# Kernel optimization log

Hardware: AMD Instinct MI355X
Metric: run time of the kernel (lower is better)

Reference implementation:

```python
import jax, jax.numpy as jnp
import numpy as np

NEG_SLOPE = 0.2
BN_EPS = 1e-5


def _gat_conv(x, src, dst, W, a_src, a_dst, b, n_nodes):
    # PyG GATConv, heads=1: linear, per-edge leaky-relu score, per-dst softmax, scatter-add.
    h = x @ W  # [N, C]
    e = jax.nn.leaky_relu((h @ a_src)[src] + (h @ a_dst)[dst], NEG_SLOPE)  # [E]
    m = jax.ops.segment_max(e, dst, num_segments=n_nodes)
    m = jnp.where(jnp.isfinite(m), m, 0.0)  # nodes with no in-edges
    w = jnp.exp(e - m[dst])
    denom = jax.ops.segment_sum(w, dst, num_segments=n_nodes)
    alpha = w / (denom[dst] + 1e-16)  # [E]
    out = jax.ops.segment_sum(alpha[:, None] * h[src], dst, num_segments=n_nodes)
    return out + b


def setup_inputs() -> dict:
    key = jax.random.key(0)
    N, E, Q, C = 50000, 800000, 200000, 128
    ks = jax.random.split(key, 12)
    sc = 1.0 / np.sqrt(C)
    d = {
        "embedding": jax.random.normal(ks[0], (N, C), jnp.float32) * 0.1,
        "W1": jax.random.normal(ks[1], (C, C), jnp.float32) * sc,
        "a_src1": jax.random.normal(ks[2], (C,), jnp.float32) * sc,
        "a_dst1": jax.random.normal(ks[3], (C,), jnp.float32) * sc,
        "b1": jnp.zeros((C,), jnp.float32),
        "gamma": jnp.ones((C,), jnp.float32),
        "beta": jnp.zeros((C,), jnp.float32),
        "rmean": jnp.zeros((C,), jnp.float32),
        "rvar": jnp.ones((C,), jnp.float32),
        "W2": jax.random.normal(ks[4], (C, C), jnp.float32) * sc,
        "a_src2": jax.random.normal(ks[5], (C,), jnp.float32) * sc,
        "a_dst2": jax.random.normal(ks[6], (C,), jnp.float32) * sc,
        "b2": jnp.zeros((C,), jnp.float32),
        "Wp1": jax.random.normal(ks[7], (C, C), jnp.float32) * sc,
        "bp1": jnp.zeros((C,), jnp.float32),
        "Wp2": jax.random.normal(ks[8], (C, 1), jnp.float32) * sc,
        "bp2": jnp.zeros((1,), jnp.float32),
        "edge_index": jax.random.randint(ks[9], (2, E), 0, N, jnp.int32),
        "edges": jax.random.randint(ks[10], (2, Q), 0, N, jnp.int32),
    }
    return d


def reference(embedding, W1, a_src1, a_dst1, b1, gamma, beta, rmean, rvar,
              W2, a_src2, a_dst2, b2, Wp1, bp1, Wp2, bp2, edge_index, edges):
    N = embedding.shape[0]
    src, dst = edge_index[0], edge_index[1]
    # conv0 -> BN (eval, running stats) -> ReLU (dropout inactive in eval)
    x = _gat_conv(embedding, src, dst, W1, a_src1, a_dst1, b1, N)
    x = (x - rmean) * jax.lax.rsqrt(rvar + BN_EPS) * gamma + beta
    x = jax.nn.relu(x)
    # final conv
    x = _gat_conv(x, src, dst, W2, a_src2, a_dst2, b2, N)
    # LinkPredictor: elementwise product of endpoint embeddings -> MLP -> sigmoid
    h = x[edges[0]] * x[edges[1]]  # [Q, C]
    h = jax.nn.relu(h @ Wp1 + bp1)
    out = jax.nn.sigmoid(h @ Wp2 + bp2)
    return out[:, 0]
```

## Files before the change

kernel.cpp:

```cpp
#include <hip/hip_runtime.h>
#include <hip/hip_bf16.h>
#include <math.h>
#include <stdint.h>
#include <string.h>

#define NEG_SLOPE 0.2f
#define BN_EPS 1e-5f

typedef __attribute__((ext_vector_type(8))) short short8;
typedef __attribute__((ext_vector_type(4))) float float4v;

static __device__ __forceinline__ unsigned short f2bf(float f) {
    union { float f; unsigned u; } v; v.f = f;
    unsigned r = (v.u + 0x7fffu + ((v.u >> 16) & 1u)) >> 16;
    return (unsigned short)r;
}
static __device__ __forceinline__ float bf2f(unsigned short u) {
    union { unsigned u; float f; } v; v.u = ((unsigned)u) << 16;
    return v.f;
}

__global__ __launch_bounds__(256) void prep_all(
    const float* __restrict__ W1, const float* __restrict__ W2,
    const float* __restrict__ Wp1,
    unsigned short* __restrict__ wt1, unsigned short* __restrict__ wt2,
    unsigned short* __restrict__ wtp,
    const float* __restrict__ gamma, const float* __restrict__ beta,
    const float* __restrict__ rmean, const float* __restrict__ rvar,
    float* __restrict__ bnsc, float* __restrict__ bnsh,
    int* __restrict__ bcur, int nz) {
    int b = blockIdx.x;
    if (b < 192) {
        const float* W = (b < 64) ? W1 : (b < 128) ? W2 : Wp1;
        unsigned short* WT = (b < 64) ? wt1 : (b < 128) ? wt2 : wtp;
        int idx = (b & 63) * 256 + threadIdx.x;
        int k = idx >> 7, n = idx & 127;
        WT[n * 128 + k] = f2bf(W[idx]);
    } else {
        if (threadIdx.x < 128) {
            int c = threadIdx.x;
            float s = gamma[c] * rsqrtf(rvar[c] + BN_EPS);
            bnsc[c] = s;
            bnsh[c] = beta[c] - rmean[c] * s;
        }
        for (int i = threadIdx.x; i < nz; i += 256) bcur[i] = 0;
    }
}

#define BK_CAP 8192
#define BK_EPB 4096
#define BK_LDS 6144

__global__ __launch_bounds__(256) void bucket_scatter(const int* __restrict__ src,
                                                      const int* __restrict__ dst,
                                                      int* __restrict__ bcur,
                                                      unsigned long long* __restrict__ bucket,
                                                      int E) {
    __shared__ int lcnt[256];
    __shared__ int lbase[256];
    int t = threadIdx.x;
    int e0 = blockIdx.x * BK_EPB;
    lcnt[t] = 0;
    __syncthreads();

    int es[16], ed[16];
#pragma unroll
    for (int u = 0; u < 16; ++u) {
        int i = e0 + u * 256 + t;
        if (i < E) {
            es[u] = src[i];
            ed[u] = dst[i];
            atomicAdd(&lcnt[ed[u] >> 8], 1);
        } else {
            ed[u] = -1;
        }
    }
    __syncthreads();
    int c = lcnt[t];
    if (c > 0) lbase[t] = atomicAdd(&bcur[t], c);
    __syncthreads();
    lcnt[t] = 0;
    __syncthreads();
#pragma unroll
    for (int u = 0; u < 16; ++u) {
        if (ed[u] >= 0) {
            int bin = ed[u] >> 8;
            int r = atomicAdd(&lcnt[bin], 1);
            int slot = lbase[bin] + r;
            if (slot < BK_CAP)
                bucket[(size_t)bin * BK_CAP + slot] =
                    ((unsigned long long)(ed[u] & 255) << 32) | (unsigned)es[u];
        }
    }
}

__global__ __launch_bounds__(256) void bucket_offs_fill(
    const int* __restrict__ bcur,
    const unsigned long long* __restrict__ bucket,
    int* __restrict__ gcnt,
    int* __restrict__ offs, int* __restrict__ ends,
    int* __restrict__ csr, int N) {
    __shared__ unsigned long long rec[BK_LDS];
    __shared__ int cnt[256];
    __shared__ int sc[256];
    __shared__ int bbase;
    int t = threadIdx.x, b = blockIdx.x;
    const unsigned long long* gb = &bucket[(size_t)b * BK_CAP];
    cnt[t] = 0;
    int c = bcur[b];
    if (c > BK_CAP) c = BK_CAP;
    if (t == 0) bbase = atomicAdd(gcnt, c);
    int lim = (c < BK_LDS) ? c : BK_LDS;
    for (int i = t; i < lim; i += 256) rec[i] = gb[i];
    __syncthreads();
    for (int i = t; i < c; i += 256) {
        unsigned long long v = (i < BK_LDS) ? rec[i] : gb[i];
        atomicAdd(&cnt[(int)(v >> 32)], 1);
    }
    __syncthreads();
    int v = cnt[t];
    sc[t] = v;
    __syncthreads();
    for (int d = 1; d < 256; d <<= 1) {
        int u = (t >= d) ? sc[t - d] : 0;
        __syncthreads();
        sc[t] += u;
        __syncthreads();
    }
    int myoff = bbase + sc[t] - v;
    int node = (b << 8) + t;
    if (node < N) {
        offs[node] = myoff;
        ends[node] = myoff + v;
    }
    cnt[t] = myoff;
    __syncthreads();
    for (int i = t; i < c; i += 256) {
        unsigned long long rv = (i < BK_LDS) ? rec[i] : gb[i];
        int dl = (int)(rv >> 32);
        int s = (int)(rv & 0xffffffffu);
        int r = atomicAdd(&cnt[dl], 1);
        csr[r] = s;
    }
}

#define LP_RS 136

template <bool BF16_IN>
__global__ __launch_bounds__(256) void gemm_mfma(
    const void* __restrict__ Xv,
    const unsigned short* __restrict__ WT,
    const float* __restrict__ a_src, const float* __restrict__ a_dst,
    unsigned short* __restrict__ H,
    float* __restrict__ s_src, float* __restrict__ s_dst, int N)
{
    __shared__ unsigned short sA[128 * LP_RS];
    __shared__ unsigned short sW[128 * LP_RS];
    const float* Xf = (const float*)Xv;
    const unsigned short* Xh = (const unsigned short*)Xv;
    int tid = threadIdx.x;
    int r0 = blockIdx.x * 128;

#pragma unroll
    for (int it = 0; it < 8; ++it) {
        int idx = it * 2048 + tid * 8;
        int n = idx >> 7, k = idx & 127;
        *(short8*)&sW[n * LP_RS + k] = *(const short8*)&WT[idx];
    }
#pragma unroll
    for (int it = 0; it < 16; ++it) {
        int r = it * 8 + (tid >> 5);
        int c = (tid & 31) * 4;
        int row = r0 + r;
        ushort4 u = make_ushort4(0, 0, 0, 0);
        if (row < N) {
            if (BF16_IN) {
                u = *(const ushort4*)&Xh[(size_t)row * 128 + c];
            } else {
                float4 x = *(const float4*)&Xf[(size_t)row * 128 + c];
                u.x = f2bf(x.x); u.y = f2bf(x.y); u.z = f2bf(x.z); u.w = f2bf(x.w);
            }
        }
        *(ushort4*)&sA[r * LP_RS + c] = u;
    }
    __syncthreads();

    int wave = tid >> 6, lane = tid & 63;
    int ln = lane & 15, quad = lane >> 4;
    int rowbase = wave * 32;

    short8 af[2][4];
#pragma unroll
    for (int m = 0; m < 2; ++m)
#pragma unroll
        for (int kt = 0; kt < 4; ++kt)
            af[m][kt] = *(const short8*)&sA[(rowbase + m * 16 + ln) * LP_RS + kt * 32 + quad * 8];

    float4v acc[2][8];
#pragma unroll
    for (int m = 0; m < 2; ++m)
#pragma unroll
        for (int n = 0; n < 8; ++n)
            acc[m][n] = float4v{0.f, 0.f, 0.f, 0.f};

#pragma unroll
    for (int n = 0; n < 8; ++n) {
#pragma unroll
        for (int kt = 0; kt < 4; ++kt) {
            short8 bf = *(const short8*)&sW[(n * 16 + ln) * LP_RS + kt * 32 + quad * 8];
            acc[0][n] = __builtin_amdgcn_mfma_f32_16x16x32_bf16(af[0][kt], bf, acc[0][n], 0, 0, 0);
            acc[1][n] = __builtin_amdgcn_mfma_f32_16x16x32_bf16(af[1][kt], bf, acc[1][n], 0, 0, 0);
        }
    }

    float asr[8], adr[8];
#pragma unroll
    for (int n = 0; n < 8; ++n) {
        asr[n] = a_src[n * 16 + ln];
        adr[n] = a_dst[n * 16 + ln];
    }
#pragma unroll
    for (int m = 0; m < 2; ++m) {
        int rb = r0 + rowbase + m * 16 + quad * 4;
#pragma unroll
        for (int n = 0; n < 8; ++n) {
            int col = n * 16 + ln;
            float4v a = acc[m][n];
            if (rb + 0 < N) H[(size_t)(rb + 0) * 128 + col] = f2bf(a[0]);
            if (rb + 1 < N) H[(size_t)(rb + 1) * 128 + col] = f2bf(a[1]);
            if (rb + 2 < N) H[(size_t)(rb + 2) * 128 + col] = f2bf(a[2]);
            if (rb + 3 < N) H[(size_t)(rb + 3) * 128 + col] = f2bf(a[3]);
        }
#pragma unroll
        for (int r = 0; r < 4; ++r) {
            float ps = 0.f, pd = 0.f;
#pragma unroll
            for (int n = 0; n < 8; ++n) {
                float v = acc[m][n][r];
                ps = fmaf(v, asr[n], ps);
                pd = fmaf(v, adr[n], pd);
            }
#pragma unroll
            for (int o = 1; o < 16; o <<= 1) {
                ps += __shfl_xor(ps, o);
                pd += __shfl_xor(pd, o);
            }
            int row = rb + r;
            if (ln == 0 && row < N) { s_src[row] = ps; s_dst[row] = pd; }
        }
    }
}

__global__ __launch_bounds__(256) void gat_gather(const unsigned short* __restrict__ H,
                                                  const int* __restrict__ offs,
                                                  const int* __restrict__ ends,
                                                  const int* __restrict__ csr,
                                                  const float* __restrict__ s_src,
                                                  const float* __restrict__ s_dst,
                                                  const float* __restrict__ bias,
                                                  const float* __restrict__ bn_scale,
                                                  const float* __restrict__ bn_shift,
                                                  int do_bn_relu,
                                                  unsigned short* __restrict__ out, int N) {
    int wave = threadIdx.x >> 6, lane = threadIdx.x & 63;
    int half = lane >> 5, hl = lane & 31;
    int node = blockIdx.x * 8 + wave * 2 + half;
    if (node >= N) return;
    int c0 = hl * 4;
    int beg = offs[node], end = ends[node];
    float sd = s_dst[node];

    float a0 = 0.f, a1 = 0.f, a2 = 0.f, a3 = 0.f;
    float sw = 0.f;
    for (int chunk = beg; chunk < end; chunk += 32) {
        int i = chunk + hl;
        int sidx = 0;
        float w = 0.f;
        if (i < end) {
            sidx = csr[i];
            float e = s_src[sidx] + sd;
            e = (e >= 0.f) ? e : NEG_SLOPE * e;
            w = expf(e);
        }
        sw += w;
        int cnt = end - chunk;
        if (cnt > 32) cnt = 32;
        int u = 0;
        for (; u + 8 <= cnt; u += 8) {
            int s[8]; float ww[8]; ushort4 hv[8];
#pragma unroll
            for (int j = 0; j < 8; ++j) {
                s[j]  = __shfl(sidx, u + j, 32);
                ww[j] = __shfl(w, u + j, 32);
            }
#pragma unroll
            for (int j = 0; j < 8; ++j)
                hv[j] = *(const ushort4*)&H[(size_t)s[j] * 128 + c0];
#pragma unroll
            for (int j = 0; j < 8; ++j) {
                a0 = fmaf(ww[j], bf2f(hv[j].x), a0);
                a1 = fmaf(ww[j], bf2f(hv[j].y), a1);
                a2 = fmaf(ww[j], bf2f(hv[j].z), a2);
                a3 = fmaf(ww[j], bf2f(hv[j].w), a3);
            }
        }
        for (; u + 4 <= cnt; u += 4) {
            int s[4]; float ww[4]; ushort4 hv[4];
#pragma unroll
            for (int j = 0; j < 4; ++j) {
                s[j]  = __shfl(sidx, u + j, 32);
                ww[j] = __shfl(w, u + j, 32);
            }
#pragma unroll
            for (int j = 0; j < 4; ++j)
                hv[j] = *(const ushort4*)&H[(size_t)s[j] * 128 + c0];
#pragma unroll
            for (int j = 0; j < 4; ++j) {
                a0 = fmaf(ww[j], bf2f(hv[j].x), a0);
                a1 = fmaf(ww[j], bf2f(hv[j].y), a1);
                a2 = fmaf(ww[j], bf2f(hv[j].z), a2);
                a3 = fmaf(ww[j], bf2f(hv[j].w), a3);
            }
        }
        for (; u < cnt; ++u) {
            int sj = __shfl(sidx, u, 32);
            float wj = __shfl(w, u, 32);
            ushort4 hv = *(const ushort4*)&H[(size_t)sj * 128 + c0];
            a0 = fmaf(wj, bf2f(hv.x), a0);
            a1 = fmaf(wj, bf2f(hv.y), a1);
            a2 = fmaf(wj, bf2f(hv.z), a2);
            a3 = fmaf(wj, bf2f(hv.w), a3);
        }
    }
#pragma unroll
    for (int o = 16; o; o >>= 1) sw += __shfl_xor(sw, o);
    float inv = 1.f / (sw + 1e-16f);

    float o0 = a0 * inv + bias[c0 + 0];
    float o1 = a1 * inv + bias[c0 + 1];
    float o2 = a2 * inv + bias[c0 + 2];
    float o3 = a3 * inv + bias[c0 + 3];
    if (do_bn_relu) {
        o0 = fmaxf(o0 * bn_scale[c0 + 0] + bn_shift[c0 + 0], 0.f);
        o1 = fmaxf(o1 * bn_scale[c0 + 1] + bn_shift[c0 + 1], 0.f);
        o2 = fmaxf(o2 * bn_scale[c0 + 2] + bn_shift[c0 + 2], 0.f);
        o3 = fmaxf(o3 * bn_scale[c0 + 3] + bn_shift[c0 + 3], 0.f);
    }
    ushort4 ov;
    ov.x = f2bf(o0); ov.y = f2bf(o1); ov.z = f2bf(o2); ov.w = f2bf(o3);
    *(ushort4*)&out[(size_t)node * 128 + c0] = ov;
}

__global__ __launch_bounds__(512) void link_pred_mfma(
    const unsigned short* __restrict__ X,
    const int* __restrict__ E0, const int* __restrict__ E1,
    const unsigned short* __restrict__ WTg,
    const float* __restrict__ bp1,
    const float* __restrict__ Wp2,
    const float* __restrict__ bp2_p,
    float* __restrict__ out, int Q)
{
    __shared__ unsigned short sW[128 * LP_RS];
    int tid = threadIdx.x;
    int wave = tid >> 6, lane = tid & 63;
    int ln = lane & 15, quad = lane >> 4;

    int tile = blockIdx.x * 8 + wave;
    int qbase = tile * 32;

    int ea[2], eb[2];
#pragma unroll
    for (int m = 0; m < 2; ++m) {
        int q = qbase + m * 16 + ln;
        if (q >= Q) q = Q - 1;
        ea[m] = E0[q];
        eb[m] = E1[q];
    }

#pragma unroll
    for (int it = 0; it < 4; ++it) {
        int idx = it * 4096 + tid * 8;
        int n = idx >> 7, k = idx & 127;
        *(short8*)&sW[n * LP_RS + k] = *(const short8*)&WTg[idx];
    }

    short8 ra[2][4], rb[2][4];
#pragma unroll
    for (int m = 0; m < 2; ++m) {
        const unsigned short* pa = &X[(size_t)ea[m] * 128 + quad * 8];
        const unsigned short* pb = &X[(size_t)eb[m] * 128 + quad * 8];
#pragma unroll
        for (int kt = 0; kt < 4; ++kt) {
            ra[m][kt] = *(const short8*)(pa + kt * 32);
            rb[m][kt] = *(const short8*)(pb + kt * 32);
        }
    }

    float bias[8], w2c[8];
#pragma unroll
    for (int n = 0; n < 8; ++n) {
        bias[n] = bp1[n * 16 + ln];
        w2c[n] = Wp2[n * 16 + ln];
    }
    float b2 = bp2_p[0];

    __syncthreads();

    short8 af[2][4];
#pragma unroll
    for (int m = 0; m < 2; ++m) {
#pragma unroll
        for (int kt = 0; kt < 4; ++kt) {
            short8 p;
#pragma unroll
            for (int j = 0; j < 8; j += 2) {
                float p0 = bf2f((unsigned short)ra[m][kt][j]) *
                           bf2f((unsigned short)rb[m][kt][j]);
                float p1 = bf2f((unsigned short)ra[m][kt][j + 1]) *
                           bf2f((unsigned short)rb[m][kt][j + 1]);
                __hip_bfloat162 h2 = __float22bfloat162_rn(make_float2(p0, p1));
                unsigned pr;
                memcpy(&pr, &h2, 4);
                p[j]     = (short)(pr & 0xffffu);
                p[j + 1] = (short)(pr >> 16);
            }
            af[m][kt] = p;
        }
    }

    float r0[2] = {0.f, 0.f}, r1[2] = {0.f, 0.f}, r2[2] = {0.f, 0.f}, r3[2] = {0.f, 0.f};
#pragma unroll
    for (int n = 0; n < 8; ++n) {
        float4v a0 = float4v{bias[n], bias[n], bias[n], bias[n]};
        float4v a1 = a0;
#pragma unroll
        for (int kt = 0; kt < 4; ++kt) {
            short8 bf = *(const short8*)&sW[(n * 16 + ln) * LP_RS + kt * 32 + quad * 8];
            a0 = __builtin_amdgcn_mfma_f32_16x16x32_bf16(af[0][kt], bf, a0, 0, 0, 0);
            a1 = __builtin_amdgcn_mfma_f32_16x16x32_bf16(af[1][kt], bf, a1, 0, 0, 0);
        }
        float w = w2c[n];
        r0[0] += fmaxf(a0[0], 0.f) * w;  r0[1] += fmaxf(a1[0], 0.f) * w;
        r1[0] += fmaxf(a0[1], 0.f) * w;  r1[1] += fmaxf(a1[1], 0.f) * w;
        r2[0] += fmaxf(a0[2], 0.f) * w;  r2[1] += fmaxf(a1[2], 0.f) * w;
        r3[0] += fmaxf(a0[3], 0.f) * w;  r3[1] += fmaxf(a1[3], 0.f) * w;
    }
#pragma unroll
    for (int m = 0; m < 2; ++m) {
#pragma unroll
        for (int o = 1; o < 16; o <<= 1) {
            r0[m] += __shfl_xor(r0[m], o);
            r1[m] += __shfl_xor(r1[m], o);
            r2[m] += __shfl_xor(r2[m], o);
            r3[m] += __shfl_xor(r3[m], o);
        }
        if (ln == 0) {
            int rbase = qbase + m * 16 + quad * 4;
            float rv[4] = {r0[m], r1[m], r2[m], r3[m]};
#pragma unroll
            for (int r = 0; r < 4; ++r) {
                int q = rbase + r;
                if (q < Q) out[q] = 1.f / (1.f + expf(-(rv[r] + b2)));
            }
        }
    }
}

extern "C" void kernel_launch(void* const* d_in, const int* in_sizes, int n_in,
                              void* d_out, int out_size, void* d_ws, size_t ws_size,
                              hipStream_t stream) {
    const float* emb    = (const float*)d_in[0];
    const float* W1     = (const float*)d_in[1];
    const float* a_src1 = (const float*)d_in[2];
    const float* a_dst1 = (const float*)d_in[3];
    const float* b1     = (const float*)d_in[4];
    const float* gamma  = (const float*)d_in[5];
    const float* beta   = (const float*)d_in[6];
    const float* rmean  = (const float*)d_in[7];
    const float* rvar   = (const float*)d_in[8];
    const float* W2     = (const float*)d_in[9];
    const float* a_src2 = (const float*)d_in[10];
    const float* a_dst2 = (const float*)d_in[11];
    const float* b2     = (const float*)d_in[12];
    const float* Wp1    = (const float*)d_in[13];
    const float* bp1    = (const float*)d_in[14];
    const float* Wp2    = (const float*)d_in[15];
    const float* bp2    = (const float*)d_in[16];
    const int* edge_index = (const int*)d_in[17];
    const int* edges      = (const int*)d_in[18];

    const int N = in_sizes[0] / 128;
    const int E = in_sizes[17] / 2;
    const int Q = in_sizes[18] / 2;
    const int* src = edge_index;
    const int* dst = edge_index + E;
    const int* e0 = edges;
    const int* e1 = edges + Q;
    float* out = (float*)d_out;

    uintptr_t base = (uintptr_t)d_ws;
    size_t cur = 0;
    auto take = [&](size_t bytes) -> void* {
        void* p = (void*)(base + cur);
        cur += (bytes + 255) & ~(size_t)255;
        return p;
    };
    unsigned short* bufA = (unsigned short*)take((size_t)N * 128 * 2);
    unsigned short* bufB = (unsigned short*)take((size_t)N * 128 * 2);
    float* s_src  = (float*)take((size_t)N * 4);
    float* s_dst  = (float*)take((size_t)N * 4);
    float* bnsc   = (float*)take(128 * 4);
    float* bnsh   = (float*)take(128 * 4);
    int*   offs   = (int*)take((size_t)N * 4);
    int*   ends   = (int*)take((size_t)N * 4);
    int*   csr    = (int*)take((size_t)E * 4);
    unsigned short* wt1 = (unsigned short*)take(128 * 128 * 2);
    unsigned short* wt2 = (unsigned short*)take(128 * 128 * 2);
    unsigned short* wtp = (unsigned short*)take(128 * 128 * 2);
    int nb = (N + 255) / 256;
    int*   bcur   = (int*)take((size_t)(nb + 1) * 4);
    unsigned long long* bucket =
        (unsigned long long*)take((size_t)nb * BK_CAP * 8);
    (void)ws_size; (void)n_in; (void)out_size;

    prep_all<<<193, 256, 0, stream>>>(W1, W2, Wp1, wt1, wt2, wtp,
                                      gamma, beta, rmean, rvar, bnsc, bnsh,
                                      bcur, nb + 1);

    bucket_scatter<<<(E + BK_EPB - 1) / BK_EPB, 256, 0, stream>>>(src, dst, bcur, bucket, E);
    bucket_offs_fill<<<nb, 256, 0, stream>>>(bcur, bucket, &bcur[nb], offs, ends, csr, N);

    int gblk = (N + 127) / 128;
    gemm_mfma<false><<<gblk, 256, 0, stream>>>(emb, wt1, a_src1, a_dst1, bufA, s_src, s_dst, N);
    gat_gather<<<(N + 7) / 8, 256, 0, stream>>>(bufA, offs, ends, csr, s_src, s_dst,
                                                b1, bnsc, bnsh, 1, bufB, N);
    gemm_mfma<true><<<gblk, 256, 0, stream>>>(bufB, wt2, a_src2, a_dst2, bufA, s_src, s_dst, N);
    gat_gather<<<(N + 7) / 8, 256, 0, stream>>>(bufA, offs, ends, csr, s_src, s_dst,
                                                b2, nullptr, nullptr, 0, bufB, N);
    int ntiles = (Q + 31) / 32;
    int lblk = (ntiles + 7) / 8;
    link_pred_mfma<<<lblk, 512, 0, stream>>>(bufB, e0, e1, wtp, bp1, Wp2, bp2, out, Q);
}
```

Baseline: 248.0 us.

## Merge prep with bucket scatter, fuse CSR fill into first GEMM, pack bucket records

Weight/BN prep and the edge bucket scatter now run in one launch, and the CSR fill runs as extra blocks of the first GEMM launch. This drops two kernel launches and lets independent work share the GPU. Bucket records shrink from 64-bit to 32-bit (8-bit local dst, 24-bit src), halving bucket traffic and letting the whole bucket fit in LDS. A small zero_init kernel is added, and the packing assumes source ids below 2^24.

```diff
diff --git a/kernel.cpp b/kernel.cpp
--- a/kernel.cpp
+++ b/kernel.cpp
@@ -20,46 +20,21 @@
     return v.f;
 }
 
-__global__ __launch_bounds__(256) void prep_all(
-    const float* __restrict__ W1, const float* __restrict__ W2,
-    const float* __restrict__ Wp1,
-    unsigned short* __restrict__ wt1, unsigned short* __restrict__ wt2,
-    unsigned short* __restrict__ wtp,
-    const float* __restrict__ gamma, const float* __restrict__ beta,
-    const float* __restrict__ rmean, const float* __restrict__ rvar,
-    float* __restrict__ bnsc, float* __restrict__ bnsh,
-    int* __restrict__ bcur, int nz) {
-    int b = blockIdx.x;
-    if (b < 192) {
-        const float* W = (b < 64) ? W1 : (b < 128) ? W2 : Wp1;
-        unsigned short* WT = (b < 64) ? wt1 : (b < 128) ? wt2 : wtp;
-        int idx = (b & 63) * 256 + threadIdx.x;
-        int k = idx >> 7, n = idx & 127;
-        WT[n * 128 + k] = f2bf(W[idx]);
-    } else {
-        if (threadIdx.x < 128) {
-            int c = threadIdx.x;
-            float s = gamma[c] * rsqrtf(rvar[c] + BN_EPS);
-            bnsc[c] = s;
-            bnsh[c] = beta[c] - rmean[c] * s;
-        }
-        for (int i = threadIdx.x; i < nz; i += 256) bcur[i] = 0;
-    }
-}
-
 #define BK_CAP 8192
 #define BK_EPB 4096
-#define BK_LDS 6144
-
-__global__ __launch_bounds__(256) void bucket_scatter(const int* __restrict__ src,
-                                                      const int* __restrict__ dst,
-                                                      int* __restrict__ bcur,
-                                                      unsigned long long* __restrict__ bucket,
-                                                      int E) {
-    __shared__ int lcnt[256];
-    __shared__ int lbase[256];
+#define LP_RS 136
+
+__global__ __launch_bounds__(256) void zero_init(int* __restrict__ p, int n) {
+    int i = threadIdx.x + blockIdx.x * 256;
+    if (i < n) p[i] = 0;
+}
+
+static __device__ __forceinline__ void scatter_body(
+    int* lcnt, int* lbase, int blk,
+    const int* __restrict__ src, const int* __restrict__ dst,
+    int* __restrict__ bcur, unsigned int* __restrict__ bucket, int E) {
     int t = threadIdx.x;
-    int e0 = blockIdx.x * BK_EPB;
+    int e0 = blk * BK_EPB;
     lcnt[t] = 0;
     __syncthreads();
 
@@ -89,34 +64,62 @@
             int slot = lbase[bin] + r;
             if (slot < BK_CAP)
                 bucket[(size_t)bin * BK_CAP + slot] =
-                    ((unsigned long long)(ed[u] & 255) << 32) | (unsigned)es[u];
-        }
-    }
-}
-
-__global__ __launch_bounds__(256) void bucket_offs_fill(
-    const int* __restrict__ bcur,
-    const unsigned long long* __restrict__ bucket,
+                    ((unsigned)(ed[u] & 255) << 24) | (unsigned)es[u];
+        }
+    }
+}
+
+__global__ __launch_bounds__(256) void prep_scatter(
+    const float* __restrict__ W1, const float* __restrict__ W2,
+    const float* __restrict__ Wp1,
+    unsigned short* __restrict__ wt1, unsigned short* __restrict__ wt2,
+    unsigned short* __restrict__ wtp,
+    const float* __restrict__ gamma, const float* __restrict__ beta,
+    const float* __restrict__ rmean, const float* __restrict__ rvar,
+    float* __restrict__ bnsc, float* __restrict__ bnsh,
+    const int* __restrict__ src, const int* __restrict__ dst,
+    int* __restrict__ bcur, unsigned int* __restrict__ bucket, int E) {
+    __shared__ int lcnt[256];
+    __shared__ int lbase[256];
+    int b = blockIdx.x;
+    if (b < 192) {
+        const float* W = (b < 64) ? W1 : (b < 128) ? W2 : Wp1;
+        unsigned short* WT = (b < 64) ? wt1 : (b < 128) ? wt2 : wtp;
+        int idx = (b & 63) * 256 + threadIdx.x;
+        int k = idx >> 7, n = idx & 127;
+        WT[n * 128 + k] = f2bf(W[idx]);
+    } else if (b == 192) {
+        if (threadIdx.x < 128) {
+            int c = threadIdx.x;
+            float s = gamma[c] * rsqrtf(rvar[c] + BN_EPS);
+            bnsc[c] = s;
+            bnsh[c] = beta[c] - rmean[c] * s;
+        }
+    } else {
+        scatter_body(lcnt, lbase, b - 193, src, dst, bcur, bucket, E);
+    }
+}
+
+static __device__ __forceinline__ void fill_body(
+    char* base, int b,
+    const int* __restrict__ bcur, const unsigned int* __restrict__ bucket,
     int* __restrict__ gcnt,
     int* __restrict__ offs, int* __restrict__ ends,
     int* __restrict__ csr, int N) {
-    __shared__ unsigned long long rec[BK_LDS];
-    __shared__ int cnt[256];
-    __shared__ int sc[256];
-    __shared__ int bbase;
-    int t = threadIdx.x, b = blockIdx.x;
-    const unsigned long long* gb = &bucket[(size_t)b * BK_CAP];
+    unsigned int* rec = (unsigned int*)base;
+    int* cnt = (int*)(base + BK_CAP * 4);
+    int* sc  = cnt + 256;
+    int* pb  = sc + 256;
+    int t = threadIdx.x;
+    const unsigned int* gb = &bucket[(size_t)b * BK_CAP];
     cnt[t] = 0;
     int c = bcur[b];
+    if (c < 0) c = 0;
     if (c > BK_CAP) c = BK_CAP;
-    if (t == 0) bbase = atomicAdd(gcnt, c);
-    int lim = (c < BK_LDS) ? c : BK_LDS;
-    for (int i = t; i < lim; i += 256) rec[i] = gb[i];
-    __syncthreads();
-    for (int i = t; i < c; i += 256) {
-        unsigned long long v = (i < BK_LDS) ? rec[i] : gb[i];
-        atomicAdd(&cnt[(int)(v >> 32)], 1);
-    }
+    if (t == 0) *pb = atomicAdd(gcnt, c);
+    for (int i = t; i < c; i += 256) rec[i] = gb[i];
+    __syncthreads();
+    for (int i = t; i < c; i += 256) atomicAdd(&cnt[rec[i] >> 24], 1);
     __syncthreads();
     int v = cnt[t];
     sc[t] = v;
@@ -127,7 +130,7 @@
         sc[t] += u;
         __syncthreads();
     }
-    int myoff = bbase + sc[t] - v;
+    int myoff = *pb + sc[t] - v;
     int node = (b << 8) + t;
     if (node < N) {
         offs[node] = myoff;
@@ -136,30 +139,25 @@
     cnt[t] = myoff;
     __syncthreads();
     for (int i = t; i < c; i += 256) {
-        unsigned long long rv = (i < BK_LDS) ? rec[i] : gb[i];
-        int dl = (int)(rv >> 32);
-        int s = (int)(rv & 0xffffffffu);
-        int r = atomicAdd(&cnt[dl], 1);
-        csr[r] = s;
-    }
-}
-
-#define LP_RS 136
+        unsigned int rv = rec[i];
+        int r = atomicAdd(&cnt[rv >> 24], 1);
+        csr[r] = (int)(rv & 0xffffffu);
+    }
+}
 
 template <bool BF16_IN>
-__global__ __launch_bounds__(256) void gemm_mfma(
+static __device__ __forceinline__ void gemm_body(
+    unsigned short* sA, unsigned short* sW, int bid,
     const void* __restrict__ Xv,
     const unsigned short* __restrict__ WT,
     const float* __restrict__ a_src, const float* __restrict__ a_dst,
     unsigned short* __restrict__ H,
     float* __restrict__ s_src, float* __restrict__ s_dst, int N)
 {
-    __shared__ unsigned short sA[128 * LP_RS];
-    __shared__ unsigned short sW[128 * LP_RS];
     const float* Xf = (const float*)Xv;
     const unsigned short* Xh = (const unsigned short*)Xv;
     int tid = threadIdx.x;
-    int r0 = blockIdx.x * 128;
+    int r0 = bid * 128;
 
 #pragma unroll
     for (int it = 0; it < 8; ++it) {
@@ -249,6 +247,37 @@
             if (ln == 0 && row < N) { s_src[row] = ps; s_dst[row] = pd; }
         }
     }
+}
+
+__global__ __launch_bounds__(256) void gemm1_fill(
+    const void* __restrict__ Xv, const unsigned short* __restrict__ WT,
+    const float* __restrict__ a_src, const float* __restrict__ a_dst,
+    unsigned short* __restrict__ H, float* __restrict__ s_src,
+    float* __restrict__ s_dst, int N, int gblk,
+    const int* __restrict__ bcur, const unsigned int* __restrict__ bucket,
+    int* __restrict__ gcnt, int* __restrict__ offs, int* __restrict__ ends,
+    int* __restrict__ csr) {
+    __shared__ uint4 smem[4352];
+    int b = blockIdx.x;
+    if (b < gblk) {
+        unsigned short* sA = (unsigned short*)smem;
+        gemm_body<false>(sA, sA + 128 * LP_RS, b, Xv, WT, a_src, a_dst,
+                         H, s_src, s_dst, N);
+    } else {
+        fill_body((char*)smem, b - gblk, bcur, bucket, gcnt, offs, ends, csr, N);
+    }
+}
+
+template <bool BF16_IN>
+__global__ __launch_bounds__(256) void gemm_mfma(
+    const void* __restrict__ Xv, const unsigned short* __restrict__ WT,
+    const float* __restrict__ a_src, const float* __restrict__ a_dst,
+    unsigned short* __restrict__ H, float* __restrict__ s_src,
+    float* __restrict__ s_dst, int N) {
+    __shared__ uint4 smem[4352];
+    unsigned short* sA = (unsigned short*)smem;
+    gemm_body<BF16_IN>(sA, sA + 128 * LP_RS, blockIdx.x, Xv, WT, a_src, a_dst,
+                       H, s_src, s_dst, N);
 }
 
 __global__ __launch_bounds__(256) void gat_gather(const unsigned short* __restrict__ H,
@@ -519,19 +548,21 @@
     unsigned short* wtp = (unsigned short*)take(128 * 128 * 2);
     int nb = (N + 255) / 256;
     int*   bcur   = (int*)take((size_t)(nb + 1) * 4);
-    unsigned long long* bucket =
-        (unsigned long long*)take((size_t)nb * BK_CAP * 8);
+    unsigned int* bucket =
+        (unsigned int*)take((size_t)nb * BK_CAP * 4);
     (void)ws_size; (void)n_in; (void)out_size;
 
-    prep_all<<<193, 256, 0, stream>>>(W1, W2, Wp1, wt1, wt2, wtp,
-                                      gamma, beta, rmean, rvar, bnsc, bnsh,
-                                      bcur, nb + 1);
-
-    bucket_scatter<<<(E + BK_EPB - 1) / BK_EPB, 256, 0, stream>>>(src, dst, bcur, bucket, E);
-    bucket_offs_fill<<<nb, 256, 0, stream>>>(bcur, bucket, &bcur[nb], offs, ends, csr, N);
-
+    int nbs = (E + BK_EPB - 1) / BK_EPB;
     int gblk = (N + 127) / 128;
-    gemm_mfma<false><<<gblk, 256, 0, stream>>>(emb, wt1, a_src1, a_dst1, bufA, s_src, s_dst, N);
+
+    zero_init<<<1, 256, 0, stream>>>(bcur, nb + 1);
+    prep_scatter<<<193 + nbs, 256, 0, stream>>>(W1, W2, Wp1, wt1, wt2, wtp,
+                                                gamma, beta, rmean, rvar, bnsc, bnsh,
+                                                src, dst, bcur, bucket, E);
+    gemm1_fill<<<gblk + nb, 256, 0, stream>>>(emb, wt1, a_src1, a_dst1,
+                                              bufA, s_src, s_dst, N, gblk,
+                                              bcur, bucket, &bcur[nb],
+                                              offs, ends, csr);
     gat_gather<<<(N + 7) / 8, 256, 0, stream>>>(bufA, offs, ends, csr, s_src, s_dst,
                                                 b1, bnsc, bnsh, 1, bufB, N);
     gemm_mfma<true><<<gblk, 256, 0, stream>>>(bufB, wt2, a_src2, a_dst2, bufA, s_src, s_dst, N);
```

After: 238.2 us. 3.9% less time.
